# Kernel tuning notes

Hardware: AMD Instinct MI355X
Metric: run time of the kernel (lower is better)

## Reference

```python
import jax, jax.numpy as jnp
import numpy as np

N_ENT = 500000
N_REL = 64
E_DIM = 128
R_DIM = 128
REG_LAMBDA = 1e-5
M = 8192


def setup_inputs() -> dict:
    key = jax.random.key(0)
    k1, k2, k3, k4, k5, k6, k7 = jax.random.split(key, 7)
    # Xavier-uniform-ish init for relation_weight; normal for embeddings (nn.Embedding default)
    gain = float(np.sqrt(2.0))  # calculate_gain('relu')
    bound = gain * float(np.sqrt(6.0 / (E_DIM + R_DIM)))
    return {
        "h": jax.random.randint(k1, (M,), 0, N_ENT),
        "r": jax.random.randint(k2, (M,), 0, N_REL),
        "pos_t": jax.random.randint(k3, (M,), 0, N_ENT),
        "neg_t": jax.random.randint(k4, (M,), 0, N_ENT),
        "entity_embed": jax.random.normal(k5, (N_ENT, E_DIM), dtype=jnp.float32),
        "relation_embed": jax.random.normal(k6, (N_REL, R_DIM), dtype=jnp.float32),
        "relation_weight": jax.random.uniform(k7, (N_REL, E_DIM, R_DIM), dtype=jnp.float32, minval=-bound, maxval=bound),
    }


def _l2_norm(x):
    # sum over feature dim, halved -> shape (M,)
    return jnp.sum(x * x, axis=1) / 2.0


def reference(h, r, pos_t, neg_t, entity_embed, relation_embed, relation_weight):
    h_embed = entity_embed[h]            # (M, E)
    r_embed = relation_embed[r]          # (M, R)
    pos_t_embed = entity_embed[pos_t]    # (M, E)
    neg_t_embed = entity_embed[neg_t]    # (M, E)

    W = relation_weight[r]               # (M, E, R) relation-indexed gather
    h_vec = jnp.einsum('me,mer->mr', h_embed, W)
    pos_t_vec = jnp.einsum('me,mer->mr', pos_t_embed, W)
    neg_t_vec = jnp.einsum('me,mer->mr', neg_t_embed, W)

    pos_score = _l2_norm(h_vec + r_embed - pos_t_vec)
    neg_score = _l2_norm(h_vec + r_embed - neg_t_vec)
    kg_loss = jnp.mean(-jax.nn.log_sigmoid(pos_score - neg_score))

    kg_reg_loss = (jnp.mean(_l2_norm(h_embed)) + jnp.mean(_l2_norm(r_embed))
                   + jnp.mean(_l2_norm(pos_t_embed)) + jnp.mean(_l2_norm(neg_t_embed)))
    return kg_loss + REG_LAMBDA * kg_reg_loss
```

## Files before the change

kernel.cpp:

```cpp
#include <hip/hip_runtime.h>
#include <math.h>

#define E_DIM 128
#define R_DIM 128
#define N_REL 64
#define REG_LAMBDA 1e-5f

#define NSEG 16
#define G 4
#define LISTMAX 256

__global__ void __launch_bounds__(256)
kge_grouped4(const int* __restrict__ h_idx, const int* __restrict__ r_idx,
             const int* __restrict__ pt_idx, const int* __restrict__ nt_idx,
             const float* __restrict__ ent,
             const float* __restrict__ rel,
             const float* __restrict__ W,
             float* __restrict__ per_sample,
             int M)
{
    const int t      = threadIdx.x;
    const int rel_id = blockIdx.x >> 4;
    const int seg    = blockIdx.x & (NSEG - 1);
    const int q      = t >> 6;
    const int u      = t & 63;
    const int cb     = u << 1;

    __shared__ int s_cnt;
    __shared__ int s_list[LISTMAX];
    __shared__ __align__(16) float sh[G][E_DIM];
    __shared__ __align__(16) float sp[G][E_DIM];
    __shared__ __align__(16) float sn[G][E_DIM];
    __shared__ __align__(16) float epi[G][3][4][R_DIM];
    __shared__ float wpart[3][G][2];

    const int range = (M + NSEG - 1) / NSEG;
    const int m0 = seg * range;
    const int m1 = min(m0 + range, M);

    if (t == 0) s_cnt = 0;
    __syncthreads();
    for (int m = m0 + t; m < m1; m += 256) {
        if (r_idx[m] == rel_id) {
            int p = atomicAdd(&s_cnt, 1);
            if (p < LISTMAX) s_list[p] = m;
        }
    }
    __syncthreads();
    const int cnt = min(s_cnt, LISTMAX);
    if (cnt == 0) return;

    const float* __restrict__ Wq =
        W + (size_t)rel_id * (E_DIM * R_DIM) + (size_t)(q << 5) * R_DIM + cb;
    const float re = (t < E_DIM) ? rel[(size_t)rel_id * R_DIM + t] : 0.f;

    const int elem = t & 127;
    const int half = t >> 7;

    for (int c0 = 0; c0 < cnt; c0 += G) {
        for (int g = half; g < G; g += 2) {
            int sl = c0 + g; if (sl > cnt - 1) sl = cnt - 1;
            int m = s_list[sl];
            sh[g][elem] = ent[(size_t)h_idx[m]  * E_DIM + elem];
            sp[g][elem] = ent[(size_t)pt_idx[m] * E_DIM + elem];
            sn[g][elem] = ent[(size_t)nt_idx[m] * E_DIM + elem];
        }
        __syncthreads();

        float aH[G][2], aP[G][2], aN[G][2];
#pragma unroll
        for (int g = 0; g < G; ++g) {
            aH[g][0] = 0.f; aH[g][1] = 0.f;
            aP[g][0] = 0.f; aP[g][1] = 0.f;
            aN[g][0] = 0.f; aN[g][1] = 0.f;
        }

        const int eBase = q << 5;
#pragma unroll 2
        for (int es = 0; es < 8; ++es) {
            const int e0 = eBase + (es << 2);
            const float2 w0 = *(const float2*)(Wq + (size_t)((es << 2) + 0) * R_DIM);
            const float2 w1 = *(const float2*)(Wq + (size_t)((es << 2) + 1) * R_DIM);
            const float2 w2 = *(const float2*)(Wq + (size_t)((es << 2) + 2) * R_DIM);
            const float2 w3 = *(const float2*)(Wq + (size_t)((es << 2) + 3) * R_DIM);
#pragma unroll
            for (int g = 0; g < G; ++g) {
                const float4 h4 = *(const float4*)&sh[g][e0];
                const float4 p4 = *(const float4*)&sp[g][e0];
                const float4 n4 = *(const float4*)&sn[g][e0];
                aH[g][0] = fmaf(h4.x, w0.x, aH[g][0]);
                aH[g][0] = fmaf(h4.y, w1.x, aH[g][0]);
                aH[g][0] = fmaf(h4.z, w2.x, aH[g][0]);
                aH[g][0] = fmaf(h4.w, w3.x, aH[g][0]);
                aH[g][1] = fmaf(h4.x, w0.y, aH[g][1]);
                aH[g][1] = fmaf(h4.y, w1.y, aH[g][1]);
                aH[g][1] = fmaf(h4.z, w2.y, aH[g][1]);
                aH[g][1] = fmaf(h4.w, w3.y, aH[g][1]);
                aP[g][0] = fmaf(p4.x, w0.x, aP[g][0]);
                aP[g][0] = fmaf(p4.y, w1.x, aP[g][0]);
                aP[g][0] = fmaf(p4.z, w2.x, aP[g][0]);
                aP[g][0] = fmaf(p4.w, w3.x, aP[g][0]);
                aP[g][1] = fmaf(p4.x, w0.y, aP[g][1]);
                aP[g][1] = fmaf(p4.y, w1.y, aP[g][1]);
                aP[g][1] = fmaf(p4.z, w2.y, aP[g][1]);
                aP[g][1] = fmaf(p4.w, w3.y, aP[g][1]);
                aN[g][0] = fmaf(n4.x, w0.x, aN[g][0]);
                aN[g][0] = fmaf(n4.y, w1.x, aN[g][0]);
                aN[g][0] = fmaf(n4.z, w2.x, aN[g][0]);
                aN[g][0] = fmaf(n4.w, w3.x, aN[g][0]);
                aN[g][1] = fmaf(n4.x, w0.y, aN[g][1]);
                aN[g][1] = fmaf(n4.y, w1.y, aN[g][1]);
                aN[g][1] = fmaf(n4.z, w2.y, aN[g][1]);
                aN[g][1] = fmaf(n4.w, w3.y, aN[g][1]);
            }
        }

#pragma unroll
        for (int g = 0; g < G; ++g) {
            *(float2*)&epi[g][0][q][cb] = make_float2(aH[g][0], aH[g][1]);
            *(float2*)&epi[g][1][q][cb] = make_float2(aP[g][0], aP[g][1]);
            *(float2*)&epi[g][2][q][cb] = make_float2(aN[g][0], aN[g][1]);
        }
        __syncthreads();

        if (t < E_DIM) {
#pragma unroll
            for (int g = 0; g < G; ++g) {
                float hv = (epi[g][0][0][t] + epi[g][0][1][t]) + (epi[g][0][2][t] + epi[g][0][3][t]);
                float pv = (epi[g][1][0][t] + epi[g][1][1][t]) + (epi[g][1][2][t] + epi[g][1][3][t]);
                float nv = (epi[g][2][0][t] + epi[g][2][1][t]) + (epi[g][2][2][t] + epi[g][2][3][t]);
                float he = sh[g][t], pe = sp[g][t], ne = sn[g][t];
                float a  = hv + re;
                float dp = a - pv;
                float dn = a - nv;
                float pos = dp * dp;
                float neg = dn * dn;
                float reg = he * he + re * re + pe * pe + ne * ne;
#pragma unroll
                for (int off = 32; off > 0; off >>= 1) {
                    pos += __shfl_down(pos, off);
                    neg += __shfl_down(neg, off);
                    reg += __shfl_down(reg, off);
                }
                if ((t & 63) == 0) {
                    wpart[0][g][t >> 6] = pos;
                    wpart[1][g][t >> 6] = neg;
                    wpart[2][g][t >> 6] = reg;
                }
            }
        }
        __syncthreads();

        if (t < G && (c0 + t) < cnt) {
            float P  = wpart[0][t][0] + wpart[0][t][1];
            float Nn = wpart[1][t][0] + wpart[1][t][1];
            float R  = wpart[2][t][0] + wpart[2][t][1];
            float diff = 0.5f * (P - Nn);
            float z = -diff;
            float sp_v = fmaxf(z, 0.f) + log1pf(expf(-fabsf(z)));
            per_sample[s_list[c0 + t]] = sp_v + REG_LAMBDA * 0.5f * R;
        }
    }
}

__global__ void __launch_bounds__(256)
kge_reduce_kernel(const float* __restrict__ per_sample, float* __restrict__ out, int M)
{
    int t = threadIdx.x;
    float s = 0.f;
    for (int i = t; i < M; i += 256) s += per_sample[i];
#pragma unroll
    for (int off = 32; off > 0; off >>= 1) s += __shfl_down(s, off);
    __shared__ float part[4];
    if ((t & 63) == 0) part[t >> 6] = s;
    __syncthreads();
    if (t == 0) out[0] = (part[0] + part[1] + part[2] + part[3]) / (float)M;
}

extern "C" void kernel_launch(void* const* d_in, const int* in_sizes, int n_in,
                              void* d_out, int out_size, void* d_ws, size_t ws_size,
                              hipStream_t stream)
{
    const int*   h_idx  = (const int*)d_in[0];
    const int*   r_idx  = (const int*)d_in[1];
    const int*   pt_idx = (const int*)d_in[2];
    const int*   nt_idx = (const int*)d_in[3];
    const float* ent    = (const float*)d_in[4];
    const float* rel    = (const float*)d_in[5];
    const float* W      = (const float*)d_in[6];
    float* out = (float*)d_out;

    int M = in_sizes[0];
    float* per_sample = (float*)d_ws;

    kge_grouped4<<<N_REL * NSEG, 256, 0, stream>>>(h_idx, r_idx, pt_idx, nt_idx,
                                                   ent, rel, W, per_sample, M);
    kge_reduce_kernel<<<1, 256, 0, stream>>>(per_sample, out, M);
}
```

Measured before the change: 340.8 us.

## Bucket samples by relation in a sort kernel and launch one block per chunk

Adds a single-block counting sort that groups sample indices by relation and emits chunk descriptors of up to 8 samples each. The main kernel then launches one block per chunk instead of 16 segment-scanning blocks per relation that loop over their lists serially. The goal is to remove the redundant scans of r_idx and the load imbalance across blocks, at the cost of an extra serial single-block launch and dependent indirection. The group size also rises from 4 to 8, reusing each W load across more samples.

```diff
diff --git a/kernel.cpp b/kernel.cpp
--- a/kernel.cpp
+++ b/kernel.cpp
@@ -5,131 +5,170 @@
 #define R_DIM 128
 #define N_REL 64
 #define REG_LAMBDA 1e-5f
-
-#define NSEG 16
-#define G 4
-#define LISTMAX 256
-
-__global__ void __launch_bounds__(256)
-kge_grouped4(const int* __restrict__ h_idx, const int* __restrict__ r_idx,
-             const int* __restrict__ pt_idx, const int* __restrict__ nt_idx,
-             const float* __restrict__ ent,
-             const float* __restrict__ rel,
-             const float* __restrict__ W,
-             float* __restrict__ per_sample,
-             int M)
-{
-    const int t      = threadIdx.x;
-    const int rel_id = blockIdx.x >> 4;
-    const int seg    = blockIdx.x & (NSEG - 1);
-    const int q      = t >> 6;
-    const int u      = t & 63;
-    const int cb     = u << 1;
-
-    __shared__ int s_cnt;
-    __shared__ int s_list[LISTMAX];
+#define G 8
+
+__global__ void __launch_bounds__(1024)
+kge_sort_kernel(const int* __restrict__ r_idx, int M,
+                int* __restrict__ sorted, int2* __restrict__ desc,
+                int* __restrict__ nchunks_out)
+{
+    const int t = threadIdx.x;
+    __shared__ int hist[N_REL], base[N_REL], cursor[N_REL];
+    __shared__ int s_total;
+
+    if (t < N_REL) { hist[t] = 0; cursor[t] = 0; }
+    __syncthreads();
+
+    for (int m = t; m < M; m += 1024) atomicAdd(&hist[r_idx[m]], 1);
+    __syncthreads();
+
+    if (t < N_REL) {
+        const int c = hist[t];
+        int x = c;
+#pragma unroll
+        for (int off = 1; off < 64; off <<= 1) {
+            int y = __shfl_up(x, off);
+            if (t >= off) x += y;
+        }
+        base[t] = x - c;
+        const int nch = (c + G - 1) / G;
+        int z = nch;
+#pragma unroll
+        for (int off = 1; off < 64; off <<= 1) {
+            int y = __shfl_up(z, off);
+            if (t >= off) z += y;
+        }
+        const int cb = z - nch;
+        if (t == N_REL - 1) s_total = z;
+        for (int j = 0; j < nch; ++j) {
+            int len = c - j * G; if (len > G) len = G;
+            desc[cb + j] = make_int2((x - c) + j * G, (t << 16) | len);
+        }
+    }
+    __syncthreads();
+
+    for (int m = t; m < M; m += 1024) {
+        int r = r_idx[m];
+        int p = base[r] + atomicAdd(&cursor[r], 1);
+        sorted[p] = m;
+    }
+    if (t == 0) nchunks_out[0] = s_total;
+}
+
+__global__ void __launch_bounds__(256, 4)
+kge_chunk_kernel(const int* __restrict__ sorted, const int2* __restrict__ desc,
+                 const int* __restrict__ nchunks_ptr,
+                 const int* __restrict__ h_idx, const int* __restrict__ pt_idx,
+                 const int* __restrict__ nt_idx,
+                 const float* __restrict__ ent,
+                 const float* __restrict__ rel,
+                 const float* __restrict__ W,
+                 float* __restrict__ per_sample)
+{
+    const int bid = blockIdx.x;
+    if (bid >= nchunks_ptr[0]) return;
+    const int2 d     = desc[bid];
+    const int start  = d.x;
+    const int rel_id = d.y >> 16;
+    const int len    = d.y & 0xffff;
+
+    const int t  = threadIdx.x;
+    const int q  = t >> 6;
+    const int u  = t & 63;
+    const int cb = u << 1;
+
     __shared__ __align__(16) float sh[G][E_DIM];
     __shared__ __align__(16) float sp[G][E_DIM];
     __shared__ __align__(16) float sn[G][E_DIM];
-    __shared__ __align__(16) float epi[G][3][4][R_DIM];
+    __shared__ __align__(16) float epi[4][3][4][R_DIM];
     __shared__ float wpart[3][G][2];
-
-    const int range = (M + NSEG - 1) / NSEG;
-    const int m0 = seg * range;
-    const int m1 = min(m0 + range, M);
-
-    if (t == 0) s_cnt = 0;
-    __syncthreads();
-    for (int m = m0 + t; m < m1; m += 256) {
-        if (r_idx[m] == rel_id) {
-            int p = atomicAdd(&s_cnt, 1);
-            if (p < LISTMAX) s_list[p] = m;
-        }
-    }
-    __syncthreads();
-    const int cnt = min(s_cnt, LISTMAX);
-    if (cnt == 0) return;
+    __shared__ int s_ids[G];
+
+    if (t < G) s_ids[t] = sorted[start + min(t, len - 1)];
+    __syncthreads();
+
+    const int elem = t & 127;
+    const int half = t >> 7;
+    for (int g = half; g < G; g += 2) {
+        int m = s_ids[g];
+        sh[g][elem] = ent[(size_t)h_idx[m]  * E_DIM + elem];
+        sp[g][elem] = ent[(size_t)pt_idx[m] * E_DIM + elem];
+        sn[g][elem] = ent[(size_t)nt_idx[m] * E_DIM + elem];
+    }
+    __syncthreads();
 
     const float* __restrict__ Wq =
         W + (size_t)rel_id * (E_DIM * R_DIM) + (size_t)(q << 5) * R_DIM + cb;
     const float re = (t < E_DIM) ? rel[(size_t)rel_id * R_DIM + t] : 0.f;
 
-    const int elem = t & 127;
-    const int half = t >> 7;
-
-    for (int c0 = 0; c0 < cnt; c0 += G) {
-        for (int g = half; g < G; g += 2) {
-            int sl = c0 + g; if (sl > cnt - 1) sl = cnt - 1;
-            int m = s_list[sl];
-            sh[g][elem] = ent[(size_t)h_idx[m]  * E_DIM + elem];
-            sp[g][elem] = ent[(size_t)pt_idx[m] * E_DIM + elem];
-            sn[g][elem] = ent[(size_t)nt_idx[m] * E_DIM + elem];
+    float aH[G][2], aP[G][2], aN[G][2];
+#pragma unroll
+    for (int g = 0; g < G; ++g) {
+        aH[g][0] = 0.f; aH[g][1] = 0.f;
+        aP[g][0] = 0.f; aP[g][1] = 0.f;
+        aN[g][0] = 0.f; aN[g][1] = 0.f;
+    }
+
+    const int eBase = q << 5;
+#pragma unroll 2
+    for (int es = 0; es < 8; ++es) {
+        const int e0 = eBase + (es << 2);
+        const float2 w0 = *(const float2*)(Wq + (size_t)((es << 2) + 0) * R_DIM);
+        const float2 w1 = *(const float2*)(Wq + (size_t)((es << 2) + 1) * R_DIM);
+        const float2 w2 = *(const float2*)(Wq + (size_t)((es << 2) + 2) * R_DIM);
+        const float2 w3 = *(const float2*)(Wq + (size_t)((es << 2) + 3) * R_DIM);
+#pragma unroll
+        for (int g = 0; g < G; ++g) {
+            const float4 h4 = *(const float4*)&sh[g][e0];
+            const float4 p4 = *(const float4*)&sp[g][e0];
+            const float4 n4 = *(const float4*)&sn[g][e0];
+            aH[g][0] = fmaf(h4.x, w0.x, aH[g][0]);
+            aH[g][0] = fmaf(h4.y, w1.x, aH[g][0]);
+            aH[g][0] = fmaf(h4.z, w2.x, aH[g][0]);
+            aH[g][0] = fmaf(h4.w, w3.x, aH[g][0]);
+            aH[g][1] = fmaf(h4.x, w0.y, aH[g][1]);
+            aH[g][1] = fmaf(h4.y, w1.y, aH[g][1]);
+            aH[g][1] = fmaf(h4.z, w2.y, aH[g][1]);
+            aH[g][1] = fmaf(h4.w, w3.y, aH[g][1]);
+            aP[g][0] = fmaf(p4.x, w0.x, aP[g][0]);
+            aP[g][0] = fmaf(p4.y, w1.x, aP[g][0]);
+            aP[g][0] = fmaf(p4.z, w2.x, aP[g][0]);
+            aP[g][0] = fmaf(p4.w, w3.x, aP[g][0]);
+            aP[g][1] = fmaf(p4.x, w0.y, aP[g][1]);
+            aP[g][1] = fmaf(p4.y, w1.y, aP[g][1]);
+            aP[g][1] = fmaf(p4.z, w2.y, aP[g][1]);
+            aP[g][1] = fmaf(p4.w, w3.y, aP[g][1]);
+            aN[g][0] = fmaf(n4.x, w0.x, aN[g][0]);
+            aN[g][0] = fmaf(n4.y, w1.x, aN[g][0]);
+            aN[g][0] = fmaf(n4.z, w2.x, aN[g][0]);
+            aN[g][0] = fmaf(n4.w, w3.x, aN[g][0]);
+            aN[g][1] = fmaf(n4.x, w0.y, aN[g][1]);
+            aN[g][1] = fmaf(n4.y, w1.y, aN[g][1]);
+            aN[g][1] = fmaf(n4.z, w2.y, aN[g][1]);
+            aN[g][1] = fmaf(n4.w, w3.y, aN[g][1]);
+        }
+    }
+
+#pragma unroll
+    for (int r0 = 0; r0 < G; r0 += 4) {
+        if (r0) __syncthreads();
+#pragma unroll
+        for (int g = 0; g < 4; ++g) {
+            const int gg = r0 + g;
+            *(float2*)&epi[g][0][q][cb] = make_float2(aH[gg][0], aH[gg][1]);
+            *(float2*)&epi[g][1][q][cb] = make_float2(aP[gg][0], aP[gg][1]);
+            *(float2*)&epi[g][2][q][cb] = make_float2(aN[gg][0], aN[gg][1]);
         }
         __syncthreads();
 
-        float aH[G][2], aP[G][2], aN[G][2];
-#pragma unroll
-        for (int g = 0; g < G; ++g) {
-            aH[g][0] = 0.f; aH[g][1] = 0.f;
-            aP[g][0] = 0.f; aP[g][1] = 0.f;
-            aN[g][0] = 0.f; aN[g][1] = 0.f;
-        }
-
-        const int eBase = q << 5;
-#pragma unroll 2
-        for (int es = 0; es < 8; ++es) {
-            const int e0 = eBase + (es << 2);
-            const float2 w0 = *(const float2*)(Wq + (size_t)((es << 2) + 0) * R_DIM);
-            const float2 w1 = *(const float2*)(Wq + (size_t)((es << 2) + 1) * R_DIM);
-            const float2 w2 = *(const float2*)(Wq + (size_t)((es << 2) + 2) * R_DIM);
-            const float2 w3 = *(const float2*)(Wq + (size_t)((es << 2) + 3) * R_DIM);
-#pragma unroll
-            for (int g = 0; g < G; ++g) {
-                const float4 h4 = *(const float4*)&sh[g][e0];
-                const float4 p4 = *(const float4*)&sp[g][e0];
-                const float4 n4 = *(const float4*)&sn[g][e0];
-                aH[g][0] = fmaf(h4.x, w0.x, aH[g][0]);
-                aH[g][0] = fmaf(h4.y, w1.x, aH[g][0]);
-                aH[g][0] = fmaf(h4.z, w2.x, aH[g][0]);
-                aH[g][0] = fmaf(h4.w, w3.x, aH[g][0]);
-                aH[g][1] = fmaf(h4.x, w0.y, aH[g][1]);
-                aH[g][1] = fmaf(h4.y, w1.y, aH[g][1]);
-                aH[g][1] = fmaf(h4.z, w2.y, aH[g][1]);
-                aH[g][1] = fmaf(h4.w, w3.y, aH[g][1]);
-                aP[g][0] = fmaf(p4.x, w0.x, aP[g][0]);
-                aP[g][0] = fmaf(p4.y, w1.x, aP[g][0]);
-                aP[g][0] = fmaf(p4.z, w2.x, aP[g][0]);
-                aP[g][0] = fmaf(p4.w, w3.x, aP[g][0]);
-                aP[g][1] = fmaf(p4.x, w0.y, aP[g][1]);
-                aP[g][1] = fmaf(p4.y, w1.y, aP[g][1]);
-                aP[g][1] = fmaf(p4.z, w2.y, aP[g][1]);
-                aP[g][1] = fmaf(p4.w, w3.y, aP[g][1]);
-                aN[g][0] = fmaf(n4.x, w0.x, aN[g][0]);
-                aN[g][0] = fmaf(n4.y, w1.x, aN[g][0]);
-                aN[g][0] = fmaf(n4.z, w2.x, aN[g][0]);
-                aN[g][0] = fmaf(n4.w, w3.x, aN[g][0]);
-                aN[g][1] = fmaf(n4.x, w0.y, aN[g][1]);
-                aN[g][1] = fmaf(n4.y, w1.y, aN[g][1]);
-                aN[g][1] = fmaf(n4.z, w2.y, aN[g][1]);
-                aN[g][1] = fmaf(n4.w, w3.y, aN[g][1]);
-            }
-        }
-
-#pragma unroll
-        for (int g = 0; g < G; ++g) {
-            *(float2*)&epi[g][0][q][cb] = make_float2(aH[g][0], aH[g][1]);
-            *(float2*)&epi[g][1][q][cb] = make_float2(aP[g][0], aP[g][1]);
-            *(float2*)&epi[g][2][q][cb] = make_float2(aN[g][0], aN[g][1]);
-        }
-        __syncthreads();
-
         if (t < E_DIM) {
 #pragma unroll
-            for (int g = 0; g < G; ++g) {
+            for (int g = 0; g < 4; ++g) {
+                const int gg = r0 + g;
                 float hv = (epi[g][0][0][t] + epi[g][0][1][t]) + (epi[g][0][2][t] + epi[g][0][3][t]);
                 float pv = (epi[g][1][0][t] + epi[g][1][1][t]) + (epi[g][1][2][t] + epi[g][1][3][t]);
                 float nv = (epi[g][2][0][t] + epi[g][2][1][t]) + (epi[g][2][2][t] + epi[g][2][3][t]);
-                float he = sh[g][t], pe = sp[g][t], ne = sn[g][t];
+                float he = sh[gg][t], pe = sp[gg][t], ne = sn[gg][t];
                 float a  = hv + re;
                 float dp = a - pv;
                 float dn = a - nv;
@@ -143,23 +182,23 @@
                     reg += __shfl_down(reg, off);
                 }
                 if ((t & 63) == 0) {
-                    wpart[0][g][t >> 6] = pos;
-                    wpart[1][g][t >> 6] = neg;
-                    wpart[2][g][t >> 6] = reg;
+                    wpart[0][gg][t >> 6] = pos;
+                    wpart[1][gg][t >> 6] = neg;
+                    wpart[2][gg][t >> 6] = reg;
                 }
             }
         }
-        __syncthreads();
-
-        if (t < G && (c0 + t) < cnt) {
-            float P  = wpart[0][t][0] + wpart[0][t][1];
-            float Nn = wpart[1][t][0] + wpart[1][t][1];
-            float R  = wpart[2][t][0] + wpart[2][t][1];
-            float diff = 0.5f * (P - Nn);
-            float z = -diff;
-            float sp_v = fmaxf(z, 0.f) + log1pf(expf(-fabsf(z)));
-            per_sample[s_list[c0 + t]] = sp_v + REG_LAMBDA * 0.5f * R;
-        }
+    }
+    __syncthreads();
+
+    if (t < len) {
+        float P  = wpart[0][t][0] + wpart[0][t][1];
+        float Nn = wpart[1][t][0] + wpart[1][t][1];
+        float R  = wpart[2][t][0] + wpart[2][t][1];
+        float diff = 0.5f * (P - Nn);
+        float z = -diff;
+        float sp_v = fmaxf(z, 0.f) + log1pf(expf(-fabsf(z)));
+        per_sample[s_ids[t]] = sp_v + REG_LAMBDA * 0.5f * R;
     }
 }
 
@@ -191,9 +230,16 @@
     float* out = (float*)d_out;
 
     int M = in_sizes[0];
+    const int maxChunks = (M + G - 1) / G + N_REL;
+
     float* per_sample = (float*)d_ws;
-
-    kge_grouped4<<<N_REL * NSEG, 256, 0, stream>>>(h_idx, r_idx, pt_idx, nt_idx,
-                                                   ent, rel, W, per_sample, M);
+    int*   sorted     = (int*)(per_sample + M);
+    int2*  desc       = (int2*)(sorted + M);
+    int*   nchunks    = (int*)(desc + maxChunks);
+
+    kge_sort_kernel<<<1, 1024, 0, stream>>>(r_idx, M, sorted, desc, nchunks);
+    kge_chunk_kernel<<<maxChunks, 256, 0, stream>>>(sorted, desc, nchunks,
+                                                    h_idx, pt_idx, nt_idx,
+                                                    ent, rel, W, per_sample);
     kge_reduce_kernel<<<1, 256, 0, stream>>>(per_sample, out, M);
 }
```

After: 372.9 us. 1.09x slower.
